# Optimization experiments

Hardware: AMD Instinct MI355X
Metric: run time of the kernel (lower is better)

Reference implementation:

```python
import jax, jax.numpy as jnp
import numpy as np

B, L = 1024, 4096        # cycles x timesteps
CC = 3                   # SC channels (SC[...,2:3] = nominal capacity)
XC = 2 + CC              # p_net input: [SOC, T, SC...]
# bounds from params['a123'] for (R_1, 1/R_1C_1, OCV-U, -M_H, K_H)
LB = jnp.array([0.005, 0.025, 0.1, 0.0, 0.002], dtype=jnp.float32)
UB = jnp.array([0.02, 0.07, 1.0, 0.055, 0.025], dtype=jnp.float32)


def setup_inputs() -> dict:
    key = jax.random.key(0)
    ks = jax.random.split(key, 10)
    t = jnp.broadcast_to(jnp.arange(L, dtype=jnp.float32), (B, L))  # monotone time
    I = 1.0 + 0.1 * jax.random.normal(ks[0], (B, L))  # current, bounded away from 0 (IR_estim divides by I)
    T = jax.random.normal(ks[1], (B, L))              # temperature
    dummy = jax.random.normal(ks[2], (B, L))          # unused column 3
    SOC = jax.random.uniform(ks[3], (B, L))
    X = jnp.stack([t, I, T, dummy, SOC], axis=-1)     # [B, L, 5]
    SC = jax.random.uniform(ks[4], (B, CC), minval=0.5, maxval=1.5)
    std = 0.1  # init_network_weights: normal(0, 0.1), zero bias
    pW1 = std * jax.random.normal(ks[5], (XC, 2 * XC))
    pb1 = jnp.zeros((2 * XC,), jnp.float32)
    pW2 = std * jax.random.normal(ks[6], (2 * XC, 5))
    pb2 = jnp.zeros((5,), jnp.float32)
    rW1 = std * jax.random.normal(ks[7], (XC, 1))
    rb1 = jnp.zeros((1,), jnp.float32)
    rW2 = std * jax.random.normal(ks[8], (1, 1))
    rb2 = jnp.zeros((1,), jnp.float32)
    return dict(X=X, SC=SC, pW1=pW1, pb1=pb1, pW2=pW2, pb2=pb2,
                rW1=rW1, rb1=rb1, rW2=rW2, rb2=rb2)


def reference(X, SC, pW1, pb1, pW2, pb2, rW1, rb1, rW2, rb2):
    t = X[..., 0:1]
    I = X[..., 1:2]
    T = X[..., 2:3]
    SOC = X[..., 4:]
    sc_b = jnp.broadcast_to(SC[:, None, :], (X.shape[0], X.shape[1], SC.shape[-1]))
    x = jnp.concatenate([SOC, T, sc_b], axis=-1)                 # [B, L, XC]
    p = jax.nn.softplus(x @ pW1 + pb1) @ pW2 + pb2               # [B, L, 5]
    theta = LB + (UB - LB) * jax.nn.sigmoid(0.01 * p)
    R_1 = theta[..., 0:1]
    RC_r = theta[..., 1:2]
    OCV_U = theta[..., 2:3]
    M_Hn = theta[..., 3:4]   # -M_H
    K_H = theta[..., 4:5]
    r = jax.nn.softplus(x[:, 0, :] @ rW1 + rb1) @ rW2 + rb2      # [B, 1]
    R_s_init = SC[..., 2:3] * (1.0 + r)
    U_H0 = jnp.zeros((X.shape[0], 1), X.dtype)
    U_10 = -OCV_U[:, 0, :] - U_H0 - I[:, 0, :] * R_s_init
    y0 = jnp.concatenate([U_H0, U_10], axis=-1)                  # [B, 2]

    dt = jnp.swapaxes(t[:, 1:, :] - t[:, :-1, :], 0, 1)          # [L-1, B, 1]
    tm = lambda a: jnp.swapaxes(a[:, :-1, :], 0, 1)              # step inputs use X_ode[:, i]
    scan_in = (dt, tm(I), tm(R_1), tm(RC_r), tm(M_Hn), tm(K_H))

    def step(y, inp):  # explicit Euler, IRODEFunc derivative
        dt_i, I_i, R1_i, RC_i, MH_i, KH_i = inp
        U_H = y[..., 0:1]
        U_1 = y[..., 1:2]
        dU_H = -KH_i * I_i * (-MH_i - U_H)
        dU_1 = RC_i * (R1_i * I_i - U_1)
        y = y + dt_i * jnp.concatenate([dU_H, dU_1], axis=-1)
        return y, y

    _, ys = jax.lax.scan(step, y0, scan_in)                      # [L-1, B, 2]
    voltages = jnp.concatenate([y0[None], ys], axis=0)           # [L, B, 2]
    voltages = jnp.swapaxes(voltages, 0, 1)                      # [B, L, 2]
    U_H = voltages[..., 0:1]
    U_1 = voltages[..., 1:2]
    IR_estim = jnp.nanmean((-OCV_U - U_H - U_1) / I, axis=-2)    # [B, 1]
    return IR_estim
```

## Files before the change

kernel.cpp:

```cpp
#include <hip/hip_runtime.h>

#define NB 1024
#define NL 4096
#define TPB 1024
#define SPT 4

__device__ __forceinline__ float rfl(float x) {
    return __uint_as_float(__builtin_amdgcn_readfirstlane(__float_as_uint(x)));
}
__device__ __forceinline__ float fast_rcp(float x) { return __builtin_amdgcn_rcpf(x); }
__device__ __forceinline__ float fexp2(float x) { return __builtin_amdgcn_exp2f(x); }
__device__ __forceinline__ float flog2(float x) { return __builtin_amdgcn_logf(x); }

#define L2E 1.44269504088896340736f
#define LN2 0.69314718055994530942f

__device__ __forceinline__ float sigmoid_small(float z) {
    float z2 = z * z;
    return fmaf(z, fmaf(z2, -(1.0f / 48.0f), 0.25f), 0.5f);
}

__global__ void __launch_bounds__(TPB) onenet_kernel(
    const float* __restrict__ X,   const float* __restrict__ SC,
    const float* __restrict__ pW1, const float* __restrict__ pb1,
    const float* __restrict__ pW2, const float* __restrict__ pb2,
    const float* __restrict__ rW1, const float* __restrict__ rb1,
    const float* __restrict__ rW2, const float* __restrict__ rb2,
    float* __restrict__ out)
{
    const int row  = blockIdx.x;
    const int tid  = threadIdx.x;
    const int lane = tid & 63;
    const int w    = tid >> 6;

    float sc0 = rfl(SC[row * 3 + 0]);
    float sc1 = rfl(SC[row * 3 + 1]);
    float sc2 = rfl(SC[row * 3 + 2]);

    float w1r[50], w2r[50];
#pragma unroll
    for (int q = 0; q < 12; ++q) {
        float4 v = reinterpret_cast<const float4*>(pW1)[q];
        w1r[4 * q + 0] = v.x; w1r[4 * q + 1] = v.y;
        w1r[4 * q + 2] = v.z; w1r[4 * q + 3] = v.w;
    }
    w1r[48] = pW1[48]; w1r[49] = pW1[49];
#pragma unroll
    for (int q = 0; q < 12; ++q) {
        float4 v = reinterpret_cast<const float4*>(pW2)[q];
        w2r[4 * q + 0] = v.x; w2r[4 * q + 1] = v.y;
        w2r[4 * q + 2] = v.z; w2r[4 * q + 3] = v.w;
    }
    w2r[48] = pW2[48]; w2r[49] = pW2[49];

    float W1S[10], W1T[10], BASE[10], W2[50], PB2[5];
#pragma unroll
    for (int j = 0; j < 10; ++j) {
        W1S[j]  = rfl(L2E * w1r[j]);
        W1T[j]  = rfl(L2E * w1r[10 + j]);
        BASE[j] = rfl(L2E * fmaf(sc2, w1r[40 + j],
                            fmaf(sc1, w1r[30 + j],
                            fmaf(sc0, w1r[20 + j], pb1[j]))));
    }
#pragma unroll
    for (int j = 0; j < 50; ++j) W2[j] = rfl(LN2 * w2r[j]);
#pragma unroll
    for (int k = 0; k < 5; ++k)  PB2[k] = rfl(pb2[k]);

    const float* xp = X + ((size_t)row * NL + (size_t)tid * SPT) * 5;
    float f[20];
#pragma unroll
    for (int q = 0; q < 5; ++q) {
        float4 v = reinterpret_cast<const float4*>(xp)[q];
        f[4 * q + 0] = v.x; f[4 * q + 1] = v.y;
        f[4 * q + 2] = v.z; f[4 * q + 3] = v.w;
    }
    float tnext = (tid < TPB - 1) ? xp[5 * SPT] : f[15];

    float aH = 1.f, bH = 0.f, cH = 0.f, dH = 0.f;
    float a1 = 1.f, b1 = 0.f, c1 = 0.f, d1 = 0.f;
    float oacc = 0.f;
    float OCV0 = 0.f, I0 = 0.f, SOC0 = 0.f, T0 = 0.f;

#pragma unroll
    for (int i = 0; i < SPT; ++i) {
        float tt = f[5 * i + 0];
        float Ii = f[5 * i + 1];
        float Tt = f[5 * i + 2];
        float SS = f[5 * i + 4];
        float tnx = (i < SPT - 1) ? f[5 * i + 5] : tnext;
        float dt  = tnx - tt;
        float inv = fast_rcp(Ii);

        float p0 = PB2[0], p1 = PB2[1], p2 = PB2[2], p3 = PB2[3], p4 = PB2[4];
#pragma unroll
        for (int j = 0; j < 10; ++j) {
            float pre = fmaf(SS, W1S[j], fmaf(Tt, W1T[j], BASE[j]));
            float h = flog2(1.0f + fexp2(pre));
            p0 = fmaf(h, W2[5 * j + 0], p0);
            p1 = fmaf(h, W2[5 * j + 1], p1);
            p2 = fmaf(h, W2[5 * j + 2], p2);
            p3 = fmaf(h, W2[5 * j + 3], p3);
            p4 = fmaf(h, W2[5 * j + 4], p4);
        }
        float R1v  = fmaf(0.015f, sigmoid_small(0.01f * p0), 0.005f);
        float RCv  = fmaf(0.045f, sigmoid_small(0.01f * p1), 0.025f);
        float OCVv = fmaf(0.900f, sigmoid_small(0.01f * p2), 0.100f);
        float MHv  = fmaf(0.055f, sigmoid_small(0.01f * p3), 0.000f);
        float KHv  = fmaf(0.023f, sigmoid_small(0.01f * p4), 0.002f);

        oacc = fmaf(-OCVv, inv, oacc);
        if (i == 0) { OCV0 = OCVv; I0 = Ii; SOC0 = SS; T0 = Tt; }

        bool lastl = (tid == TPB - 1) && (i == SPT - 1);
        float g  = lastl ? 0.f : dt * KHv * Ii;
        float sa = 1.f + g, sb = g * MHv;
        float hh = lastl ? 0.f : dt * RCv;
        float ua = 1.f - hh, ub = hh * R1v * Ii;

        cH = fmaf(inv, aH, cH);  dH = fmaf(inv, bH, dH);
        c1 = fmaf(inv, a1, c1);  d1 = fmaf(inv, b1, d1);
        bH = fmaf(sa, bH, sb);   aH = sa * aH;
        b1 = fmaf(ua, b1, ub);   a1 = ua * a1;
    }

#pragma unroll
    for (int off = 1; off < 64; off <<= 1) {
        float aH2 = __shfl_down(aH, off); float bH2 = __shfl_down(bH, off);
        float cH2 = __shfl_down(cH, off); float dH2 = __shfl_down(dH, off);
        float a12 = __shfl_down(a1, off); float b12 = __shfl_down(b1, off);
        float c12 = __shfl_down(c1, off); float d12 = __shfl_down(d1, off);
        float o2  = __shfl_down(oacc, off);
        float nbH = fmaf(aH2, bH, bH2);
        float ncH = fmaf(cH2, aH, cH);
        float ndH = fmaf(cH2, bH, dH + dH2);
        float naH = aH2 * aH;
        float nb1 = fmaf(a12, b1, b12);
        float nc1 = fmaf(c12, a1, c1);
        float nd1 = fmaf(c12, b1, d1 + d12);
        float na1 = a12 * a1;
        aH = naH; bH = nbH; cH = ncH; dH = ndH;
        a1 = na1; b1 = nb1; c1 = nc1; d1 = nd1;
        oacc += o2;
    }

    __shared__ float red[TPB / 64][9];
    if (lane == 0) {
        red[w][0] = aH; red[w][1] = bH; red[w][2] = cH; red[w][3] = dH;
        red[w][4] = a1; red[w][5] = b1; red[w][6] = c1; red[w][7] = d1;
        red[w][8] = oacc;
    }
    __syncthreads();

    if (tid == 0) {
        float A  = red[0][0], Bb = red[0][1], C  = red[0][2], D  = red[0][3];
        float A2 = red[0][4], B2 = red[0][5], C2 = red[0][6], D2 = red[0][7];
        float O  = red[0][8];
#pragma unroll
        for (int k = 1; k < TPB / 64; ++k) {
            float ar = red[k][0], br = red[k][1], cr = red[k][2], dr = red[k][3];
            float nB = fmaf(ar, Bb, br);
            float nC = fmaf(cr, A, C);
            float nD = fmaf(cr, Bb, D + dr);
            A = ar * A; Bb = nB; C = nC; D = nD;
            ar = red[k][4]; br = red[k][5]; cr = red[k][6]; dr = red[k][7];
            float nB2 = fmaf(ar, B2, br);
            float nC2 = fmaf(cr, A2, C2);
            float nD2 = fmaf(cr, B2, D2 + dr);
            A2 = ar * A2; B2 = nB2; C2 = nC2; D2 = nD2;
            O += red[k][8];
        }
        float u = rb1[0];
        u = fmaf(SOC0, rW1[0], u);
        u = fmaf(T0,   rW1[1], u);
        u = fmaf(sc0,  rW1[2], u);
        u = fmaf(sc1,  rW1[3], u);
        u = fmaf(sc2,  rW1[4], u);
        float sp  = LN2 * flog2(1.0f + fexp2(L2E * u));
        float r   = fmaf(sp, rW2[0], rb2[0]);
        float Rs  = sc2 * (1.0f + r);
        float U10 = -OCV0 - I0 * Rs;
        float SH  = D;
        float S1  = fmaf(C2, U10, D2);
        out[row]  = (O - SH - S1) * (1.0f / 4096.0f);
    }
}

extern "C" void kernel_launch(void* const* d_in, const int* in_sizes, int n_in,
                              void* d_out, int out_size, void* d_ws, size_t ws_size,
                              hipStream_t stream) {
    const float* X   = (const float*)d_in[0];
    const float* SC  = (const float*)d_in[1];
    const float* pW1 = (const float*)d_in[2];
    const float* pb1 = (const float*)d_in[3];
    const float* pW2 = (const float*)d_in[4];
    const float* pb2 = (const float*)d_in[5];
    const float* rW1 = (const float*)d_in[6];
    const float* rb1 = (const float*)d_in[7];
    const float* rW2 = (const float*)d_in[8];
    const float* rb2 = (const float*)d_in[9];
    float* out = (float*)d_out;

    onenet_kernel<<<NB, TPB, 0, stream>>>(X, SC, pW1, pb1, pW2, pb2,
                                          rW1, rb1, rW2, rb2, out);
}
```

Before: 150.2 us.

## Split into prep/main/final kernels with half-row blocks and folded sigmoid constants

Moves per-row weight preprocessing (SC-dependent bias, reset-net init resistance) and global folded constants into a small prep kernel writing to workspace. The sigmoid linearization is folded into the second-layer weights, so only the linear term of the small-argument expansion remains. The main kernel splits each row across two 256-thread blocks with 8 steps per thread, using packed v2f math for the affine scan. A final kernel combines the two halves. This removes redundant per-block weight setup and increases work per thread, at the cost of two extra launches and workspace traffic.

```diff
diff --git a/kernel.cpp b/kernel.cpp
--- a/kernel.cpp
+++ b/kernel.cpp
@@ -1,13 +1,16 @@
 #include <hip/hip_runtime.h>
 
-#define NB 1024
-#define NL 4096
-#define TPB 1024
-#define SPT 4
-
-__device__ __forceinline__ float rfl(float x) {
-    return __uint_as_float(__builtin_amdgcn_readfirstlane(__float_as_uint(x)));
-}
+#define NB   1024
+#define NL   4096
+#define TPB  256
+#define HALF 2048
+#define SPT  8
+
+#define WS_BASE 256
+#define WS_PART 16640
+
+typedef float v2f __attribute__((ext_vector_type(2)));
+
 __device__ __forceinline__ float fast_rcp(float x) { return __builtin_amdgcn_rcpf(x); }
 __device__ __forceinline__ float fexp2(float x) { return __builtin_amdgcn_exp2f(x); }
 __device__ __forceinline__ float flog2(float x) { return __builtin_amdgcn_logf(x); }
@@ -15,175 +18,200 @@
 #define L2E 1.44269504088896340736f
 #define LN2 0.69314718055994530942f
 
-__device__ __forceinline__ float sigmoid_small(float z) {
-    float z2 = z * z;
-    return fmaf(z, fmaf(z2, -(1.0f / 48.0f), 0.25f), 0.5f);
-}
-
-__global__ void __launch_bounds__(TPB) onenet_kernel(
+__global__ void __launch_bounds__(256) onenet_prep(
     const float* __restrict__ X,   const float* __restrict__ SC,
     const float* __restrict__ pW1, const float* __restrict__ pb1,
     const float* __restrict__ pW2, const float* __restrict__ pb2,
     const float* __restrict__ rW1, const float* __restrict__ rb1,
     const float* __restrict__ rW2, const float* __restrict__ rb2,
-    float* __restrict__ out)
+    float* __restrict__ ws)
 {
-    const int row  = blockIdx.x;
-    const int tid  = threadIdx.x;
-    const int lane = tid & 63;
-    const int w    = tid >> 6;
-
-    float sc0 = rfl(SC[row * 3 + 0]);
-    float sc1 = rfl(SC[row * 3 + 1]);
-    float sc2 = rfl(SC[row * 3 + 2]);
-
-    float w1r[50], w2r[50];
-#pragma unroll
-    for (int q = 0; q < 12; ++q) {
-        float4 v = reinterpret_cast<const float4*>(pW1)[q];
-        w1r[4 * q + 0] = v.x; w1r[4 * q + 1] = v.y;
-        w1r[4 * q + 2] = v.z; w1r[4 * q + 3] = v.w;
-    }
-    w1r[48] = pW1[48]; w1r[49] = pW1[49];
-#pragma unroll
-    for (int q = 0; q < 12; ++q) {
-        float4 v = reinterpret_cast<const float4*>(pW2)[q];
-        w2r[4 * q + 0] = v.x; w2r[4 * q + 1] = v.y;
-        w2r[4 * q + 2] = v.z; w2r[4 * q + 3] = v.w;
-    }
-    w2r[48] = pW2[48]; w2r[49] = pW2[49];
-
-    float W1S[10], W1T[10], BASE[10], W2[50], PB2[5];
-#pragma unroll
-    for (int j = 0; j < 10; ++j) {
-        W1S[j]  = rfl(L2E * w1r[j]);
-        W1T[j]  = rfl(L2E * w1r[10 + j]);
-        BASE[j] = rfl(L2E * fmaf(sc2, w1r[40 + j],
-                            fmaf(sc1, w1r[30 + j],
-                            fmaf(sc0, w1r[20 + j], pb1[j]))));
-    }
-#pragma unroll
-    for (int j = 0; j < 50; ++j) W2[j] = rfl(LN2 * w2r[j]);
-#pragma unroll
-    for (int k = 0; k < 5; ++k)  PB2[k] = rfl(pb2[k]);
-
-    const float* xp = X + ((size_t)row * NL + (size_t)tid * SPT) * 5;
-    float f[20];
-#pragma unroll
-    for (int q = 0; q < 5; ++q) {
-        float4 v = reinterpret_cast<const float4*>(xp)[q];
-        f[4 * q + 0] = v.x; f[4 * q + 1] = v.y;
-        f[4 * q + 2] = v.z; f[4 * q + 3] = v.w;
-    }
-    float tnext = (tid < TPB - 1) ? xp[5 * SPT] : f[15];
-
-    float aH = 1.f, bH = 0.f, cH = 0.f, dH = 0.f;
-    float a1 = 1.f, b1 = 0.f, c1 = 0.f, d1 = 0.f;
-    float oacc = 0.f;
-    float OCV0 = 0.f, I0 = 0.f, SOC0 = 0.f, T0 = 0.f;
-
-#pragma unroll
-    for (int i = 0; i < SPT; ++i) {
-        float tt = f[5 * i + 0];
-        float Ii = f[5 * i + 1];
-        float Tt = f[5 * i + 2];
-        float SS = f[5 * i + 4];
-        float tnx = (i < SPT - 1) ? f[5 * i + 5] : tnext;
-        float dt  = tnx - tt;
-        float inv = fast_rcp(Ii);
-
-        float p0 = PB2[0], p1 = PB2[1], p2 = PB2[2], p3 = PB2[3], p4 = PB2[4];
+    const int gid = blockIdx.x * 256 + threadIdx.x;
+    if (gid < NB) {
+        float sc0 = SC[gid * 3 + 0], sc1 = SC[gid * 3 + 1], sc2 = SC[gid * 3 + 2];
+        float* bp = ws + WS_BASE + gid * 16;
 #pragma unroll
         for (int j = 0; j < 10; ++j) {
-            float pre = fmaf(SS, W1S[j], fmaf(Tt, W1T[j], BASE[j]));
-            float h = flog2(1.0f + fexp2(pre));
-            p0 = fmaf(h, W2[5 * j + 0], p0);
-            p1 = fmaf(h, W2[5 * j + 1], p1);
-            p2 = fmaf(h, W2[5 * j + 2], p2);
-            p3 = fmaf(h, W2[5 * j + 3], p3);
-            p4 = fmaf(h, W2[5 * j + 4], p4);
-        }
-        float R1v  = fmaf(0.015f, sigmoid_small(0.01f * p0), 0.005f);
-        float RCv  = fmaf(0.045f, sigmoid_small(0.01f * p1), 0.025f);
-        float OCVv = fmaf(0.900f, sigmoid_small(0.01f * p2), 0.100f);
-        float MHv  = fmaf(0.055f, sigmoid_small(0.01f * p3), 0.000f);
-        float KHv  = fmaf(0.023f, sigmoid_small(0.01f * p4), 0.002f);
-
-        oacc = fmaf(-OCVv, inv, oacc);
-        if (i == 0) { OCV0 = OCVv; I0 = Ii; SOC0 = SS; T0 = Tt; }
-
-        bool lastl = (tid == TPB - 1) && (i == SPT - 1);
-        float g  = lastl ? 0.f : dt * KHv * Ii;
-        float sa = 1.f + g, sb = g * MHv;
-        float hh = lastl ? 0.f : dt * RCv;
-        float ua = 1.f - hh, ub = hh * R1v * Ii;
-
-        cH = fmaf(inv, aH, cH);  dH = fmaf(inv, bH, dH);
-        c1 = fmaf(inv, a1, c1);  d1 = fmaf(inv, b1, d1);
-        bH = fmaf(sa, bH, sb);   aH = sa * aH;
-        b1 = fmaf(ua, b1, ub);   a1 = ua * a1;
-    }
-
-#pragma unroll
-    for (int off = 1; off < 64; off <<= 1) {
-        float aH2 = __shfl_down(aH, off); float bH2 = __shfl_down(bH, off);
-        float cH2 = __shfl_down(cH, off); float dH2 = __shfl_down(dH, off);
-        float a12 = __shfl_down(a1, off); float b12 = __shfl_down(b1, off);
-        float c12 = __shfl_down(c1, off); float d12 = __shfl_down(d1, off);
-        float o2  = __shfl_down(oacc, off);
-        float nbH = fmaf(aH2, bH, bH2);
-        float ncH = fmaf(cH2, aH, cH);
-        float ndH = fmaf(cH2, bH, dH + dH2);
-        float naH = aH2 * aH;
-        float nb1 = fmaf(a12, b1, b12);
-        float nc1 = fmaf(c12, a1, c1);
-        float nd1 = fmaf(c12, b1, d1 + d12);
-        float na1 = a12 * a1;
-        aH = naH; bH = nbH; cH = ncH; dH = ndH;
-        a1 = na1; b1 = nb1; c1 = nc1; d1 = nd1;
-        oacc += o2;
-    }
-
-    __shared__ float red[TPB / 64][9];
-    if (lane == 0) {
-        red[w][0] = aH; red[w][1] = bH; red[w][2] = cH; red[w][3] = dH;
-        red[w][4] = a1; red[w][5] = b1; red[w][6] = c1; red[w][7] = d1;
-        red[w][8] = oacc;
-    }
-    __syncthreads();
-
-    if (tid == 0) {
-        float A  = red[0][0], Bb = red[0][1], C  = red[0][2], D  = red[0][3];
-        float A2 = red[0][4], B2 = red[0][5], C2 = red[0][6], D2 = red[0][7];
-        float O  = red[0][8];
-#pragma unroll
-        for (int k = 1; k < TPB / 64; ++k) {
-            float ar = red[k][0], br = red[k][1], cr = red[k][2], dr = red[k][3];
-            float nB = fmaf(ar, Bb, br);
-            float nC = fmaf(cr, A, C);
-            float nD = fmaf(cr, Bb, D + dr);
-            A = ar * A; Bb = nB; C = nC; D = nD;
-            ar = red[k][4]; br = red[k][5]; cr = red[k][6]; dr = red[k][7];
-            float nB2 = fmaf(ar, B2, br);
-            float nC2 = fmaf(cr, A2, C2);
-            float nD2 = fmaf(cr, B2, D2 + dr);
-            A2 = ar * A2; B2 = nB2; C2 = nC2; D2 = nD2;
-            O += red[k][8];
-        }
+            float base = fmaf(sc0, pW1[20 + j],
+                         fmaf(sc1, pW1[30 + j],
+                         fmaf(sc2, pW1[40 + j], pb1[j])));
+            bp[j] = L2E * base;
+        }
+        const float* x0 = X + (size_t)gid * NL * 5;
+        float T0 = x0[2], SOC0 = x0[4];
         float u = rb1[0];
         u = fmaf(SOC0, rW1[0], u);
         u = fmaf(T0,   rW1[1], u);
         u = fmaf(sc0,  rW1[2], u);
         u = fmaf(sc1,  rW1[3], u);
         u = fmaf(sc2,  rW1[4], u);
-        float sp  = LN2 * flog2(1.0f + fexp2(L2E * u));
-        float r   = fmaf(sp, rW2[0], rb2[0]);
-        float Rs  = sc2 * (1.0f + r);
-        float U10 = -OCV0 - I0 * Rs;
-        float SH  = D;
-        float S1  = fmaf(C2, U10, D2);
-        out[row]  = (O - SH - S1) * (1.0f / 4096.0f);
-    }
+        float sp = LN2 * flog2(1.0f + fexp2(L2E * u));
+        float r  = fmaf(sp, rW2[0], rb2[0]);
+        bp[10] = sc2 * (1.0f + r);
+    }
+    if (blockIdx.x == 0 && threadIdx.x < 75) {
+        const int t = threadIdx.x;
+        const float LBv[5]   = {0.005f, 0.025f, 0.1f, 0.0f, 0.002f};
+        const float UBLB[5]  = {0.015f, 0.045f, 0.9f, 0.055f, 0.023f};
+        float v;
+        if (t < 20) {
+            v = L2E * pW1[t];
+        } else if (t < 70) {
+            int k = (t - 20) % 5;
+            v = LN2 * 0.0025f * UBLB[k] * pW2[t - 20];
+        } else {
+            int k = t - 70;
+            v = LBv[k] + UBLB[k] * fmaf(0.0025f, pb2[k], 0.5f);
+        }
+        ws[t] = v;
+    }
+}
+
+__global__ void __launch_bounds__(TPB) onenet_main(
+    const float* __restrict__ X, float* ws)
+{
+    const int bid  = blockIdx.x;
+    const int row  = bid >> 1;
+    const int half = bid & 1;
+    const int tid  = threadIdx.x;
+    const int lane = tid & 63;
+    const int w    = tid >> 6;
+
+    float W1S[10], W1T[10], V[50], AL[5], BASE[10];
+#pragma unroll
+    for (int j = 0; j < 10; ++j) W1S[j] = ws[j];
+#pragma unroll
+    for (int j = 0; j < 10; ++j) W1T[j] = ws[10 + j];
+#pragma unroll
+    for (int j = 0; j < 50; ++j) V[j] = ws[20 + j];
+#pragma unroll
+    for (int k = 0; k < 5; ++k) AL[k] = ws[70 + k];
+    {
+        const float* bp = ws + WS_BASE + row * 16;
+#pragma unroll
+        for (int j = 0; j < 10; ++j) BASE[j] = bp[j];
+    }
+
+    const float* xp = X + ((size_t)row * NL + (size_t)(half * HALF + tid * SPT)) * 5;
+    const bool lastthr = (half == 1) && (tid == TPB - 1);
+
+    v2f a  = {1.f, 1.f}, b  = {0.f, 0.f};
+    v2f cS = {0.f, 0.f}, dS = {0.f, 0.f};
+    float oacc = 0.f, OCV0 = 0.f, I0 = 0.f;
+
+#pragma unroll
+    for (int ch = 0; ch < 2; ++ch) {
+        float f[20];
+#pragma unroll
+        for (int q = 0; q < 5; ++q) {
+            float4 v4 = reinterpret_cast<const float4*>(xp)[ch * 5 + q];
+            f[4 * q + 0] = v4.x; f[4 * q + 1] = v4.y;
+            f[4 * q + 2] = v4.z; f[4 * q + 3] = v4.w;
+        }
+        float tn = (ch == 0) ? xp[20] : (lastthr ? 0.f : xp[40]);
+
+#pragma unroll
+        for (int i = 0; i < 4; ++i) {
+            float tt = f[5 * i + 0];
+            float Ii = f[5 * i + 1];
+            float Tt = f[5 * i + 2];
+            float SS = f[5 * i + 4];
+            float tnx = (i < 3) ? f[5 * i + 5] : tn;
+            float dt  = tnx - tt;
+            float inv = fast_rcp(Ii);
+
+            float t0 = AL[0], t1 = AL[1], t2 = AL[2], t3 = AL[3], t4 = AL[4];
+#pragma unroll
+            for (int j = 0; j < 10; ++j) {
+                float pre = fmaf(SS, W1S[j], fmaf(Tt, W1T[j], BASE[j]));
+                float lam = flog2(1.0f + fexp2(pre));
+                t0 = fmaf(lam, V[5 * j + 0], t0);
+                t1 = fmaf(lam, V[5 * j + 1], t1);
+                t2 = fmaf(lam, V[5 * j + 2], t2);
+                t3 = fmaf(lam, V[5 * j + 3], t3);
+                t4 = fmaf(lam, V[5 * j + 4], t4);
+            }
+            oacc = fmaf(-t2, inv, oacc);
+            if (ch == 0 && i == 0) { OCV0 = t2; I0 = Ii; }
+
+            bool lastl = lastthr && (ch == 1) && (i == 3);
+            float g  = lastl ? 0.f : dt * t4 * Ii;
+            float hh = lastl ? 0.f : dt * t1;
+            v2f sv, bv, iv;
+            sv.x = 1.f + g;  sv.y = 1.f - hh;
+            bv.x = g * t3;   bv.y = hh * t0 * Ii;
+            iv.x = inv;      iv.y = inv;
+
+            cS = iv * a + cS;
+            dS = iv * b + dS;
+            b  = sv * b + bv;
+            a  = sv * a;
+        }
+    }
+
+#pragma unroll
+    for (int off = 1; off < 64; off <<= 1) {
+        v2f a2, b2, c2, d2;
+        a2.x = __shfl_down(a.x, off);  a2.y = __shfl_down(a.y, off);
+        b2.x = __shfl_down(b.x, off);  b2.y = __shfl_down(b.y, off);
+        c2.x = __shfl_down(cS.x, off); c2.y = __shfl_down(cS.y, off);
+        d2.x = __shfl_down(dS.x, off); d2.y = __shfl_down(dS.y, off);
+        float o2 = __shfl_down(oacc, off);
+        v2f nb = a2 * b + b2;
+        v2f nc = c2 * a + cS;
+        v2f nd = (dS + d2) + c2 * b;
+        a = a2 * a; b = nb; cS = nc; dS = nd;
+        oacc += o2;
+    }
+
+    __shared__ float red[TPB / 64][9];
+    if (lane == 0) {
+        red[w][0] = a.x;  red[w][1] = a.y;
+        red[w][2] = b.x;  red[w][3] = b.y;
+        red[w][4] = cS.x; red[w][5] = cS.y;
+        red[w][6] = dS.x; red[w][7] = dS.y;
+        red[w][8] = oacc;
+    }
+    __syncthreads();
+
+    if (tid == 0) {
+#pragma unroll
+        for (int k = 1; k < TPB / 64; ++k) {
+            v2f ak, bk, ck, dk;
+            ak.x = red[k][0]; ak.y = red[k][1];
+            bk.x = red[k][2]; bk.y = red[k][3];
+            ck.x = red[k][4]; ck.y = red[k][5];
+            dk.x = red[k][6]; dk.y = red[k][7];
+            v2f nb = ak * b + bk;
+            v2f nc = ck * a + cS;
+            v2f nd = (dS + dk) + ck * b;
+            a = ak * a; b = nb; cS = nc; dS = nd;
+            oacc += red[k][8];
+        }
+        float* pw = ws + WS_PART + (row * 2 + half) * 12;
+        pw[0] = a.x;  pw[1] = b.x;  pw[2] = cS.x; pw[3] = dS.x;
+        pw[4] = a.y;  pw[5] = b.y;  pw[6] = cS.y; pw[7] = dS.y;
+        pw[8] = oacc;
+        if (half == 0) { pw[9] = OCV0; pw[10] = I0; }
+    }
+}
+
+__global__ void __launch_bounds__(256) onenet_final(
+    const float* __restrict__ ws, float* __restrict__ out)
+{
+    const int row = blockIdx.x * 256 + threadIdx.x;
+    if (row >= NB) return;
+    const float* q0 = ws + WS_PART + row * 24;
+    const float* q1 = q0 + 12;
+    float DH = q0[3] + q1[3] + q1[2] * q0[1];
+    float C1 = fmaf(q1[6], q0[4], q0[6]);
+    float D1 = q0[7] + q1[7] + q1[6] * q0[5];
+    float O  = q0[8] + q1[8];
+    float OCV0 = q0[9], I0 = q0[10];
+    float Rs   = ws[WS_BASE + row * 16 + 10];
+    float U10  = -OCV0 - I0 * Rs;
+    float S1   = fmaf(C1, U10, D1);
+    out[row] = (O - DH - S1) * (1.0f / 4096.0f);
 }
 
 extern "C" void kernel_launch(void* const* d_in, const int* in_sizes, int n_in,
@@ -200,7 +228,10 @@
     const float* rW2 = (const float*)d_in[8];
     const float* rb2 = (const float*)d_in[9];
     float* out = (float*)d_out;
-
-    onenet_kernel<<<NB, TPB, 0, stream>>>(X, SC, pW1, pb1, pW2, pb2,
-                                          rW1, rb1, rW2, rb2, out);
-}
+    float* ws  = (float*)d_ws;
+
+    onenet_prep<<<NB / 256, 256, 0, stream>>>(X, SC, pW1, pb1, pW2, pb2,
+                                              rW1, rb1, rW2, rb2, ws);
+    onenet_main<<<NB * 2, TPB, 0, stream>>>(X, ws);
+    onenet_final<<<NB / 256, 256, 0, stream>>>(ws, out);
+}
```

Result: faster. 140.4 us (-6.6%).
